# Kernel tuning notes

Measured on AMD Instinct MI355X. Metric: run time of the kernel, lower is better.

## Reference

```python
import jax, jax.numpy as jnp
import numpy as np

B, S, H = 2, 2048, 1024
NUM_HEAD = 16
HEAD = H // NUM_HEAD
NEG = -10000000000.0


def setup_inputs() -> dict:
    key = jax.random.key(0)
    ks = jax.random.split(key, 10)
    scale = 1.0 / np.sqrt(H)
    return {
        "query": jax.random.normal(ks[0], (B, S, H), jnp.float32),
        "key": jax.random.normal(ks[1], (B, S, H), jnp.float32),
        "value": jax.random.normal(ks[2], (B, S, H), jnp.float32),
        "mask": jax.random.randint(ks[3], (B, S), 0, 2, jnp.int32),
        "Wq": jax.random.normal(ks[4], (H, H), jnp.float32) * scale,
        "bq": jnp.zeros((H,), jnp.float32),
        "Wk": jax.random.normal(ks[5], (H, H), jnp.float32) * scale,
        "bk": jnp.zeros((H,), jnp.float32),
        "Wv": jax.random.normal(ks[6], (H, H), jnp.float32) * scale,
        "bv": jnp.zeros((H,), jnp.float32),
    }


def reference(query, key, value, mask, Wq, bq, Wk, bk, Wv, bv):
    b, s, h = query.shape
    # Linear projections (torch Linear: x @ W.T + b), split into heads -> [b, nh, s, hd]
    def proj(x, W, bias):
        y = x @ W.T + bias
        return y.reshape(b, s, NUM_HEAD, HEAD).transpose(0, 2, 1, 3)

    q = proj(query, Wq, bq)
    k = proj(key, Wk, bk)
    v = proj(value, Wv, bv)

    # NOTE: original module has NO 1/sqrt(head_dim) scaling -- faithful.
    attn_score = jnp.einsum("bhqd,bhkd->bhqk", q, k)  # [b, nh, s, s]
    # key-padding mask bias: 0 where mask==1, -1e10 where mask==0, broadcast over query dim
    bias_add = jnp.where(mask[:, None, None, :] == 0, NEG, 0.0).astype(attn_score.dtype)
    attn_score = attn_score + bias_add
    attn_ratio = jax.nn.softmax(attn_score, axis=-1)
    out = jnp.einsum("bhqk,bhkd->bhqd", attn_ratio, v)  # [b, nh, s, hd]
    out = out.transpose(0, 2, 1, 3).reshape(b, s, h)
    # Dropout is identity in eval mode; output_linear is defined but never used in forward.
    return out
```

## Files before the change

### kernel.cpp

```cpp
#include <hip/hip_runtime.h>

#define BATCH 2
#define S_LEN 2048
#define HDIM  1024
#define NHEAD 16
#define HD    64
#define NEGBIAS -1e10f

typedef __attribute__((ext_vector_type(8))) _Float16 half8;
typedef __attribute__((ext_vector_type(4))) _Float16 half4;
typedef __attribute__((ext_vector_type(4))) float   f32x4;

__global__ __launch_bounds__(256) void proj_gemm_f16(
    const float* __restrict__ Xq, const float* __restrict__ Wq, const float* __restrict__ bq,
    const float* __restrict__ Xk, const float* __restrict__ Wk, const float* __restrict__ bk,
    const float* __restrict__ Xv, const float* __restrict__ Wv, const float* __restrict__ bv,
    _Float16* __restrict__ Qb, _Float16* __restrict__ Kb, _Float16* __restrict__ Vtb)
{
    const int z = blockIdx.z;
    const float* X    = (z == 0) ? Xq : (z == 1) ? Xk : Xv;
    const float* W    = (z == 0) ? Wq : (z == 1) ? Wk : Wv;
    const float* bias = (z == 0) ? bq : (z == 1) ? bk : bv;
    _Float16* Y       = (z == 0) ? Qb : (z == 1) ? Kb : Vtb;

    const int n0 = blockIdx.x * 128;
    const int m0 = blockIdx.y * 128;

    __shared__ __align__(16) _Float16 As[128][40];
    __shared__ __align__(16) _Float16 Bs[128][40];

    const int t    = threadIdx.x;
    const int w    = t >> 6;
    const int lane = t & 63;
    const int quad = lane >> 4;
    const int lc   = lane & 15;
    const int wm   = (w >> 1) * 64;
    const int wn   = (w & 1) * 64;

    const f32x4 fzero = {0.f, 0.f, 0.f, 0.f};
    f32x4 acc[4][4];
#pragma unroll
    for (int i = 0; i < 4; i++)
#pragma unroll
        for (int j = 0; j < 4; j++) acc[i][j] = fzero;

    const int srow = t >> 2;
    const int sc   = t & 3;

    float4 xa[2][2], wa[2][2];
#define PROJ_ISSUE(K0)                                                        \
    {                                                                         \
        _Pragma("unroll")                                                     \
        for (int hf = 0; hf < 2; hf++) {                                      \
            const float* gx = X + (size_t)(m0 + srow + hf * 64) * HDIM + (K0) + sc * 8; \
            xa[hf][0] = *(const float4*)gx;                                   \
            xa[hf][1] = *(const float4*)(gx + 4);                             \
            const float* gw = W + (size_t)(n0 + srow + hf * 64) * HDIM + (K0) + sc * 8; \
            wa[hf][0] = *(const float4*)gw;                                   \
            wa[hf][1] = *(const float4*)(gw + 4);                             \
        }                                                                     \
    }

    PROJ_ISSUE(0)

    for (int k0 = 0; k0 < HDIM; k0 += 32) {
        if (k0) __syncthreads();
#pragma unroll
        for (int hf = 0; hf < 2; hf++) {
            int row = srow + hf * 64;
            half8 vx;
            vx[0] = (_Float16)xa[hf][0].x; vx[1] = (_Float16)xa[hf][0].y;
            vx[2] = (_Float16)xa[hf][0].z; vx[3] = (_Float16)xa[hf][0].w;
            vx[4] = (_Float16)xa[hf][1].x; vx[5] = (_Float16)xa[hf][1].y;
            vx[6] = (_Float16)xa[hf][1].z; vx[7] = (_Float16)xa[hf][1].w;
            *(half8*)&As[row][sc * 8] = vx;
            half8 vw;
            vw[0] = (_Float16)wa[hf][0].x; vw[1] = (_Float16)wa[hf][0].y;
            vw[2] = (_Float16)wa[hf][0].z; vw[3] = (_Float16)wa[hf][0].w;
            vw[4] = (_Float16)wa[hf][1].x; vw[5] = (_Float16)wa[hf][1].y;
            vw[6] = (_Float16)wa[hf][1].z; vw[7] = (_Float16)wa[hf][1].w;
            *(half8*)&Bs[row][sc * 8] = vw;
        }
        __syncthreads();

        if (k0 + 32 < HDIM) PROJ_ISSUE(k0 + 32)

        half8 af[4], bf[4];
#pragma unroll
        for (int mt = 0; mt < 4; mt++)
            af[mt] = *(const half8*)&As[wm + mt * 16 + lc][quad * 8];
#pragma unroll
        for (int nt = 0; nt < 4; nt++)
            bf[nt] = *(const half8*)&Bs[wn + nt * 16 + lc][quad * 8];
#pragma unroll
        for (int mt = 0; mt < 4; mt++)
#pragma unroll
            for (int nt = 0; nt < 4; nt++)
                acc[mt][nt] = __builtin_amdgcn_mfma_f32_16x16x32_f16(
                    af[mt], bf[nt], acc[mt][nt], 0, 0, 0);
    }

#pragma unroll
    for (int nt = 0; nt < 4; nt++) {
        const int n = n0 + wn + nt * 16 + lc;
        const float bv_ = bias[n];
        const int h = n >> 6, d = n & 63;
#pragma unroll
        for (int mt = 0; mt < 4; mt++) {
#pragma unroll
            for (int r = 0; r < 4; r++) {
                const int m = m0 + wm + mt * 16 + quad * 4 + r;
                const int b = m >> 11, s = m & (S_LEN - 1);
                const int bh = b * NHEAD + h;
                _Float16 val = (_Float16)(acc[mt][nt][r] + bv_);
                if (z == 2)
                    Y[((size_t)bh * HD + d) * S_LEN + s] = val;
                else
                    Y[((size_t)bh * S_LEN + s) * HD + d] = val;
            }
        }
    }
}

__global__ __launch_bounds__(256) void flash_attn_mfma(
    const _Float16* __restrict__ Qb, const _Float16* __restrict__ Kb,
    const _Float16* __restrict__ Vtb, const int* __restrict__ mask,
    float* __restrict__ out)
{
    const int qt = blockIdx.x & 15;
    const int bh = blockIdx.x >> 4;
    const int b  = bh >> 4;
    const int h  = bh & (NHEAD - 1);

    __shared__ __align__(16) _Float16 Ks [64][72];
    __shared__ __align__(16) _Float16 Vts[64][72];
    __shared__ __align__(16) _Float16 Ps [4][32][72];
    __shared__ float biasS[64];

    const int t    = threadIdx.x;
    const int w    = t >> 6;
    const int lane = t & 63;
    const int quad = lane >> 4;
    const int lc   = lane & 15;

    const _Float16* Kbase = Kb  + (size_t)bh * S_LEN * HD;
    const _Float16* Vbase = Vtb + (size_t)bh * HD * S_LEN;
    const int* mbase = mask + b * S_LEN;

    half8 qf[2][2];
#pragma unroll
    for (int qg = 0; qg < 2; qg++) {
        const int qrow = qt * 128 + w * 32 + qg * 16 + lc;
#pragma unroll
        for (int s = 0; s < 2; s++)
            qf[qg][s] = *(const half8*)(Qb + ((size_t)bh * S_LEN + qrow) * HD
                                        + s * 32 + quad * 8);
    }

    const f32x4 fzero = {0.f, 0.f, 0.f, 0.f};
    f32x4 o[2][4];
#pragma unroll
    for (int qg = 0; qg < 2; qg++)
#pragma unroll
        for (int nt = 0; nt < 4; nt++) o[qg][nt] = fzero;
    float mrun[2] = {-3.0e38f, -3.0e38f};
    float lrun[2] = {0.f, 0.f};

    const int rr0 = t >> 3,          cc0 = (t & 7) * 8;
    const int rr1 = (t + 256) >> 3,  cc1 = (t & 7) * 8;

    half8 kpre[2], vpre[2];
    int   mpre;
#define ATTN_ISSUE(KT)                                                        \
    {                                                                         \
        kpre[0] = *(const half8*)(Kbase + (size_t)((KT) + rr0) * HD + cc0);   \
        kpre[1] = *(const half8*)(Kbase + (size_t)((KT) + rr1) * HD + cc1);   \
        vpre[0] = *(const half8*)(Vbase + (size_t)rr0 * S_LEN + (KT) + cc0);  \
        vpre[1] = *(const half8*)(Vbase + (size_t)rr1 * S_LEN + (KT) + cc1);  \
        mpre    = mbase[(KT) + (t & 63)];                                     \
    }

    ATTN_ISSUE(0)

    for (int kt = 0; kt < S_LEN; kt += 64) {
        if (kt) __syncthreads();
        *(half8*)&Ks [rr0][cc0] = kpre[0];
        *(half8*)&Ks [rr1][cc1] = kpre[1];
        *(half8*)&Vts[rr0][cc0] = vpre[0];
        *(half8*)&Vts[rr1][cc1] = vpre[1];
        if (t < 64) biasS[t] = mpre ? 0.f : NEGBIAS;
        __syncthreads();

        if (kt + 64 < S_LEN) ATTN_ISSUE(kt + 64)

        f32x4 scf[2][4];
#pragma unroll
        for (int qg = 0; qg < 2; qg++)
#pragma unroll
            for (int tt = 0; tt < 4; tt++) scf[qg][tt] = fzero;
#pragma unroll
        for (int s = 0; s < 2; s++) {
#pragma unroll
            for (int tt = 0; tt < 4; tt++) {
                half8 kf = *(const half8*)&Ks[tt * 16 + lc][s * 32 + quad * 8];
                scf[0][tt] = __builtin_amdgcn_mfma_f32_16x16x32_f16(kf, qf[0][s], scf[0][tt], 0, 0, 0);
                scf[1][tt] = __builtin_amdgcn_mfma_f32_16x16x32_f16(kf, qf[1][s], scf[1][tt], 0, 0, 0);
            }
        }

#pragma unroll
        for (int tt = 0; tt < 4; tt++) {
            float4 b4 = *(const float4*)&biasS[tt * 16 + quad * 4];
#pragma unroll
            for (int qg = 0; qg < 2; qg++) {
                scf[qg][tt][0] += b4.x; scf[qg][tt][1] += b4.y;
                scf[qg][tt][2] += b4.z; scf[qg][tt][3] += b4.w;
            }
        }

#pragma unroll
        for (int qg = 0; qg < 2; qg++) {
            float mx = scf[qg][0][0];
#pragma unroll
            for (int tt = 0; tt < 4; tt++)
#pragma unroll
                for (int r = 0; r < 4; r++) mx = fmaxf(mx, scf[qg][tt][r]);
            mx = fmaxf(mx, __shfl_xor(mx, 16));
            mx = fmaxf(mx, __shfl_xor(mx, 32));

            float mn = fmaxf(mrun[qg], mx);
            float al = __expf(mrun[qg] - mn);
            float ls = 0.f;
#pragma unroll
            for (int tt = 0; tt < 4; tt++)
#pragma unroll
                for (int r = 0; r < 4; r++) {
                    float p = __expf(scf[qg][tt][r] - mn);
                    scf[qg][tt][r] = p;
                    ls += p;
                }
            ls += __shfl_xor(ls, 16);
            ls += __shfl_xor(ls, 32);
            lrun[qg] = lrun[qg] * al + ls;
            mrun[qg] = mn;
#pragma unroll
            for (int nt = 0; nt < 4; nt++) {
                o[qg][nt][0] *= al; o[qg][nt][1] *= al;
                o[qg][nt][2] *= al; o[qg][nt][3] *= al;
            }

#pragma unroll
            for (int tt = 0; tt < 4; tt++) {
                half4 pk;
                pk[0] = (_Float16)scf[qg][tt][0]; pk[1] = (_Float16)scf[qg][tt][1];
                pk[2] = (_Float16)scf[qg][tt][2]; pk[3] = (_Float16)scf[qg][tt][3];
                *(half4*)&Ps[w][qg * 16 + lc][tt * 16 + quad * 4] = pk;
            }
        }

#pragma unroll
        for (int s = 0; s < 2; s++) {
            half8 pf0 = *(const half8*)&Ps[w][lc]     [s * 32 + quad * 8];
            half8 pf1 = *(const half8*)&Ps[w][16 + lc][s * 32 + quad * 8];
#pragma unroll
            for (int nt = 0; nt < 4; nt++) {
                half8 vf = *(const half8*)&Vts[nt * 16 + lc][s * 32 + quad * 8];
                o[0][nt] = __builtin_amdgcn_mfma_f32_16x16x32_f16(vf, pf0, o[0][nt], 0, 0, 0);
                o[1][nt] = __builtin_amdgcn_mfma_f32_16x16x32_f16(vf, pf1, o[1][nt], 0, 0, 0);
            }
        }
    }

#pragma unroll
    for (int qg = 0; qg < 2; qg++) {
        const int qrow = qt * 128 + w * 32 + qg * 16 + lc;
        const float inv = 1.f / lrun[qg];
        const size_t rowb = ((size_t)b * S_LEN + qrow) * HDIM + h * HD;
#pragma unroll
        for (int nt = 0; nt < 4; nt++) {
            float4 v;
            v.x = o[qg][nt][0] * inv; v.y = o[qg][nt][1] * inv;
            v.z = o[qg][nt][2] * inv; v.w = o[qg][nt][3] * inv;
            *(float4*)&out[rowb + nt * 16 + quad * 4] = v;
        }
    }
}

extern "C" void kernel_launch(void* const* d_in, const int* in_sizes, int n_in,
                              void* d_out, int out_size, void* d_ws, size_t ws_size,
                              hipStream_t stream) {
    const float* query = (const float*)d_in[0];
    const float* key   = (const float*)d_in[1];
    const float* value = (const float*)d_in[2];
    const int*   mask  = (const int*)  d_in[3];
    const float* Wq    = (const float*)d_in[4];
    const float* bq    = (const float*)d_in[5];
    const float* Wk    = (const float*)d_in[6];
    const float* bk    = (const float*)d_in[7];
    const float* Wv    = (const float*)d_in[8];
    const float* bv    = (const float*)d_in[9];
    float* out = (float*)d_out;

    const size_t nElem = (size_t)BATCH * S_LEN * HDIM;
    if (ws_size < 3 * nElem * sizeof(_Float16)) return;
    _Float16* Qb  = (_Float16*)d_ws;
    _Float16* Kb  = Qb + nElem;
    _Float16* Vtb = Kb + nElem;

    dim3 gproj(HDIM / 128, (BATCH * S_LEN) / 128, 3);
    proj_gemm_f16<<<gproj, 256, 0, stream>>>(query, Wq, bq, key, Wk, bk,
                                             value, Wv, bv, Qb, Kb, Vtb);

    flash_attn_mfma<<<BATCH * NHEAD * (S_LEN / 128), 256, 0, stream>>>(
        Qb, Kb, Vtb, mask, out);
}
```

Measured before the change: 243.9 us.

## Use exp2 softmax with lazy rescale, swizzled LDS, and block remap in attention

Several changes land together. Q is pre-multiplied by log2(e) in the projection so softmax can use exp2f. The running-max rescale of o and l is skipped unless some row's max grows by more than 8 (a lazy rescale). The padded LDS tiles are replaced with XOR-swizzled 128-byte rows to avoid bank conflicts and save LDS. P is packed to fp16 with cvt_pkrtz, and block indices are remapped across heads. The lazy rescale lets P values reach up to 2^8 before conversion to fp16, which carries some precision risk.

```diff
diff --git a/kernel.cpp b/kernel.cpp
--- a/kernel.cpp
+++ b/kernel.cpp
@@ -6,6 +6,7 @@
 #define NHEAD 16
 #define HD    64
 #define NEGBIAS -1e10f
+#define LOG2E 1.44269504088896f
 
 typedef __attribute__((ext_vector_type(8))) _Float16 half8;
 typedef __attribute__((ext_vector_type(4))) _Float16 half4;
@@ -112,7 +113,9 @@
                 const int m = m0 + wm + mt * 16 + quad * 4 + r;
                 const int b = m >> 11, s = m & (S_LEN - 1);
                 const int bh = b * NHEAD + h;
-                _Float16 val = (_Float16)(acc[mt][nt][r] + bv_);
+                float y = acc[mt][nt][r] + bv_;
+                if (z == 0) y *= LOG2E;
+                _Float16 val = (_Float16)y;
                 if (z == 2)
                     Y[((size_t)bh * HD + d) * S_LEN + s] = val;
                 else
@@ -121,20 +124,25 @@
         }
     }
 }
+
+
+#define SWZB(row, cb) (((row) << 7) + ((cb) ^ (((row) & 7) << 4)))
 
 __global__ __launch_bounds__(256) void flash_attn_mfma(
     const _Float16* __restrict__ Qb, const _Float16* __restrict__ Kb,
     const _Float16* __restrict__ Vtb, const int* __restrict__ mask,
     float* __restrict__ out)
 {
-    const int qt = blockIdx.x & 15;
-    const int bh = blockIdx.x >> 4;
+    const int bid = blockIdx.x;
+    const int swz = (bid & 7) * 64 + (bid >> 3);
+    const int qt = swz & 15;
+    const int bh = swz >> 4;
     const int b  = bh >> 4;
     const int h  = bh & (NHEAD - 1);
 
-    __shared__ __align__(16) _Float16 Ks [64][72];
-    __shared__ __align__(16) _Float16 Vts[64][72];
-    __shared__ __align__(16) _Float16 Ps [4][32][72];
+    __shared__ __align__(16) _Float16 KsBuf [64 * 64];
+    __shared__ __align__(16) _Float16 VtsBuf[64 * 64];
+    __shared__ __align__(16) _Float16 PsBuf [4][32 * 64];
     __shared__ float biasS[64];
 
     const int t    = threadIdx.x;
@@ -143,6 +151,10 @@
     const int quad = lane >> 4;
     const int lc   = lane & 15;
 
+    char* KsB  = (char*)KsBuf;
+    char* VtsB = (char*)VtsBuf;
+    char* PsB  = (char*)PsBuf[w];
+
     const _Float16* Kbase = Kb  + (size_t)bh * S_LEN * HD;
     const _Float16* Vbase = Vtb + (size_t)bh * HD * S_LEN;
     const int* mbase = mask + b * S_LEN;
@@ -166,28 +178,28 @@
     float mrun[2] = {-3.0e38f, -3.0e38f};
     float lrun[2] = {0.f, 0.f};
 
-    const int rr0 = t >> 3,          cc0 = (t & 7) * 8;
-    const int rr1 = (t + 256) >> 3,  cc1 = (t & 7) * 8;
+    const int rr0 = t >> 3,          cb0 = (t & 7) * 16;
+    const int rr1 = (t + 256) >> 3;
 
     half8 kpre[2], vpre[2];
     int   mpre;
-#define ATTN_ISSUE(KT)                                                        \
-    {                                                                         \
-        kpre[0] = *(const half8*)(Kbase + (size_t)((KT) + rr0) * HD + cc0);   \
-        kpre[1] = *(const half8*)(Kbase + (size_t)((KT) + rr1) * HD + cc1);   \
-        vpre[0] = *(const half8*)(Vbase + (size_t)rr0 * S_LEN + (KT) + cc0);  \
-        vpre[1] = *(const half8*)(Vbase + (size_t)rr1 * S_LEN + (KT) + cc1);  \
-        mpre    = mbase[(KT) + (t & 63)];                                     \
+#define ATTN_ISSUE(KT)                                                          \
+    {                                                                           \
+        kpre[0] = *(const half8*)(Kbase + (size_t)((KT) + rr0) * HD + (cb0 >> 1)); \
+        kpre[1] = *(const half8*)(Kbase + (size_t)((KT) + rr1) * HD + (cb0 >> 1)); \
+        vpre[0] = *(const half8*)(Vbase + (size_t)rr0 * S_LEN + (KT) + (cb0 >> 1)); \
+        vpre[1] = *(const half8*)(Vbase + (size_t)rr1 * S_LEN + (KT) + (cb0 >> 1)); \
+        mpre    = mbase[(KT) + (t & 63)];                                       \
     }
 
     ATTN_ISSUE(0)
 
     for (int kt = 0; kt < S_LEN; kt += 64) {
         if (kt) __syncthreads();
-        *(half8*)&Ks [rr0][cc0] = kpre[0];
-        *(half8*)&Ks [rr1][cc1] = kpre[1];
-        *(half8*)&Vts[rr0][cc0] = vpre[0];
-        *(half8*)&Vts[rr1][cc1] = vpre[1];
+        *(half8*)(KsB  + SWZB(rr0, cb0)) = kpre[0];
+        *(half8*)(KsB  + SWZB(rr1, cb0)) = kpre[1];
+        *(half8*)(VtsB + SWZB(rr0, cb0)) = vpre[0];
+        *(half8*)(VtsB + SWZB(rr1, cb0)) = vpre[1];
         if (t < 64) biasS[t] = mpre ? 0.f : NEGBIAS;
         __syncthreads();
 
@@ -202,7 +214,7 @@
         for (int s = 0; s < 2; s++) {
 #pragma unroll
             for (int tt = 0; tt < 4; tt++) {
-                half8 kf = *(const half8*)&Ks[tt * 16 + lc][s * 32 + quad * 8];
+                half8 kf = *(const half8*)(KsB + SWZB(tt * 16 + lc, s * 64 + quad * 16));
                 scf[0][tt] = __builtin_amdgcn_mfma_f32_16x16x32_f16(kf, qf[0][s], scf[0][tt], 0, 0, 0);
                 scf[1][tt] = __builtin_amdgcn_mfma_f32_16x16x32_f16(kf, qf[1][s], scf[1][tt], 0, 0, 0);
             }
@@ -228,43 +240,47 @@
             mx = fmaxf(mx, __shfl_xor(mx, 16));
             mx = fmaxf(mx, __shfl_xor(mx, 32));
 
-            float mn = fmaxf(mrun[qg], mx);
-            float al = __expf(mrun[qg] - mn);
+            if (!__all(mx <= mrun[qg] + 8.f)) {
+                float mn = fmaxf(mrun[qg], mx);
+                float al = exp2f(mrun[qg] - mn);
+                lrun[qg] *= al;
+#pragma unroll
+                for (int nt = 0; nt < 4; nt++) {
+                    o[qg][nt][0] *= al; o[qg][nt][1] *= al;
+                    o[qg][nt][2] *= al; o[qg][nt][3] *= al;
+                }
+                mrun[qg] = mn;
+            }
+
             float ls = 0.f;
 #pragma unroll
             for (int tt = 0; tt < 4; tt++)
 #pragma unroll
                 for (int r = 0; r < 4; r++) {
-                    float p = __expf(scf[qg][tt][r] - mn);
+                    float p = exp2f(scf[qg][tt][r] - mrun[qg]);
                     scf[qg][tt][r] = p;
                     ls += p;
                 }
             ls += __shfl_xor(ls, 16);
             ls += __shfl_xor(ls, 32);
-            lrun[qg] = lrun[qg] * al + ls;
-            mrun[qg] = mn;
+            lrun[qg] += ls;
+
+#pragma unroll
+            for (int tt = 0; tt < 4; tt++) {
+                auto pk01 = __builtin_amdgcn_cvt_pkrtz(scf[qg][tt][0], scf[qg][tt][1]);
+                auto pk23 = __builtin_amdgcn_cvt_pkrtz(scf[qg][tt][2], scf[qg][tt][3]);
+                auto pk   = __builtin_shufflevector(pk01, pk23, 0, 1, 2, 3);
+                *(decltype(pk)*)(PsB + SWZB(qg * 16 + lc, tt * 32 + quad * 8)) = pk;
+            }
+        }
+
+#pragma unroll
+        for (int s = 0; s < 2; s++) {
+            half8 pf0 = *(const half8*)(PsB + SWZB(lc,      s * 64 + quad * 16));
+            half8 pf1 = *(const half8*)(PsB + SWZB(16 + lc, s * 64 + quad * 16));
 #pragma unroll
             for (int nt = 0; nt < 4; nt++) {
-                o[qg][nt][0] *= al; o[qg][nt][1] *= al;
-                o[qg][nt][2] *= al; o[qg][nt][3] *= al;
-            }
-
-#pragma unroll
-            for (int tt = 0; tt < 4; tt++) {
-                half4 pk;
-                pk[0] = (_Float16)scf[qg][tt][0]; pk[1] = (_Float16)scf[qg][tt][1];
-                pk[2] = (_Float16)scf[qg][tt][2]; pk[3] = (_Float16)scf[qg][tt][3];
-                *(half4*)&Ps[w][qg * 16 + lc][tt * 16 + quad * 4] = pk;
-            }
-        }
-
-#pragma unroll
-        for (int s = 0; s < 2; s++) {
-            half8 pf0 = *(const half8*)&Ps[w][lc]     [s * 32 + quad * 8];
-            half8 pf1 = *(const half8*)&Ps[w][16 + lc][s * 32 + quad * 8];
-#pragma unroll
-            for (int nt = 0; nt < 4; nt++) {
-                half8 vf = *(const half8*)&Vts[nt * 16 + lc][s * 32 + quad * 8];
+                half8 vf = *(const half8*)(VtsB + SWZB(nt * 16 + lc, s * 64 + quad * 16));
                 o[0][nt] = __builtin_amdgcn_mfma_f32_16x16x32_f16(vf, pf0, o[0][nt], 0, 0, 0);
                 o[1][nt] = __builtin_amdgcn_mfma_f32_16x16x32_f16(vf, pf1, o[1][nt], 0, 0, 0);
             }
```

After: 247.1 us. About the same (+1.3%).

## Use exp2 softmax with lazy rescaling, packed fp16 converts, and block swizzle

Applied to the files above, without the earlier changes.

Q is pre-scaled by log2(e) in the projection epilogue so the softmax can use hardware exp2 directly. The running-max rescale of the output accumulators is skipped unless some lane's max grows by more than 8, and the mask bias is folded into the MFMA accumulator initialisation. Float-to-half conversions now use packed round-toward-zero instructions, max reduction uses three-input max, and attention blocks are swizzled in their launch order. The lazy rescale allows partially stale maxima, which bounds exp2 inputs near 2^8 and relies on fp16 range. Round-toward-zero also changes rounding of the P values and the projection outputs.

```diff
diff --git a/kernel.cpp b/kernel.cpp
--- a/kernel.cpp
+++ b/kernel.cpp
@@ -6,10 +6,18 @@
 #define NHEAD 16
 #define HD    64
 #define NEGBIAS -1e10f
+#define LOG2E 1.44269504088896f
 
 typedef __attribute__((ext_vector_type(8))) _Float16 half8;
 typedef __attribute__((ext_vector_type(4))) _Float16 half4;
 typedef __attribute__((ext_vector_type(4))) float   f32x4;
+typedef __attribute__((ext_vector_type(2))) __fp16 fp16x2;
+typedef __attribute__((ext_vector_type(4))) __fp16 fp16x4;
+typedef __attribute__((ext_vector_type(8))) __fp16 fp16x8;
+
+__device__ __forceinline__ float max3f(float a, float b, float c) {
+    return fmaxf(fmaxf(a, b), c);
+}
 
 __global__ __launch_bounds__(256) void proj_gemm_f16(
     const float* __restrict__ Xq, const float* __restrict__ Wq, const float* __restrict__ bq,
@@ -61,6 +69,18 @@
         }                                                                     \
     }
 
+#define PK8(dst, f0, f1)                                                      \
+    {                                                                         \
+        fp16x2 p0 = __builtin_amdgcn_cvt_pkrtz((f0).x, (f0).y);               \
+        fp16x2 p1 = __builtin_amdgcn_cvt_pkrtz((f0).z, (f0).w);               \
+        fp16x2 p2 = __builtin_amdgcn_cvt_pkrtz((f1).x, (f1).y);               \
+        fp16x2 p3 = __builtin_amdgcn_cvt_pkrtz((f1).z, (f1).w);               \
+        fp16x4 lo = __builtin_shufflevector(p0, p1, 0, 1, 2, 3);              \
+        fp16x4 hi = __builtin_shufflevector(p2, p3, 0, 1, 2, 3);              \
+        fp16x8 v8 = __builtin_shufflevector(lo, hi, 0, 1, 2, 3, 4, 5, 6, 7);  \
+        dst = __builtin_bit_cast(half8, v8);                                  \
+    }
+
     PROJ_ISSUE(0)
 
     for (int k0 = 0; k0 < HDIM; k0 += 32) {
@@ -68,17 +88,10 @@
 #pragma unroll
         for (int hf = 0; hf < 2; hf++) {
             int row = srow + hf * 64;
-            half8 vx;
-            vx[0] = (_Float16)xa[hf][0].x; vx[1] = (_Float16)xa[hf][0].y;
-            vx[2] = (_Float16)xa[hf][0].z; vx[3] = (_Float16)xa[hf][0].w;
-            vx[4] = (_Float16)xa[hf][1].x; vx[5] = (_Float16)xa[hf][1].y;
-            vx[6] = (_Float16)xa[hf][1].z; vx[7] = (_Float16)xa[hf][1].w;
+            half8 vx, vw;
+            PK8(vx, xa[hf][0], xa[hf][1])
+            PK8(vw, wa[hf][0], wa[hf][1])
             *(half8*)&As[row][sc * 8] = vx;
-            half8 vw;
-            vw[0] = (_Float16)wa[hf][0].x; vw[1] = (_Float16)wa[hf][0].y;
-            vw[2] = (_Float16)wa[hf][0].z; vw[3] = (_Float16)wa[hf][0].w;
-            vw[4] = (_Float16)wa[hf][1].x; vw[5] = (_Float16)wa[hf][1].y;
-            vw[6] = (_Float16)wa[hf][1].z; vw[7] = (_Float16)wa[hf][1].w;
             *(half8*)&Bs[row][sc * 8] = vw;
         }
         __syncthreads();
@@ -112,7 +125,9 @@
                 const int m = m0 + wm + mt * 16 + quad * 4 + r;
                 const int b = m >> 11, s = m & (S_LEN - 1);
                 const int bh = b * NHEAD + h;
-                _Float16 val = (_Float16)(acc[mt][nt][r] + bv_);
+                float y = acc[mt][nt][r] + bv_;
+                if (z == 0) y *= LOG2E;
+                _Float16 val = (_Float16)y;
                 if (z == 2)
                     Y[((size_t)bh * HD + d) * S_LEN + s] = val;
                 else
@@ -127,8 +142,10 @@
     const _Float16* __restrict__ Vtb, const int* __restrict__ mask,
     float* __restrict__ out)
 {
-    const int qt = blockIdx.x & 15;
-    const int bh = blockIdx.x >> 4;
+    const int bid = blockIdx.x;
+    const int swz = (bid & 7) * 64 + (bid >> 3);
+    const int qt = swz & 15;
+    const int bh = swz >> 4;
     const int b  = bh >> 4;
     const int h  = bh & (NHEAD - 1);
 
@@ -157,8 +174,8 @@
                                         + s * 32 + quad * 8);
     }
 
+    f32x4 o[2][4];
     const f32x4 fzero = {0.f, 0.f, 0.f, 0.f};
-    f32x4 o[2][4];
 #pragma unroll
     for (int qg = 0; qg < 2; qg++)
 #pragma unroll
@@ -167,16 +184,16 @@
     float lrun[2] = {0.f, 0.f};
 
     const int rr0 = t >> 3,          cc0 = (t & 7) * 8;
-    const int rr1 = (t + 256) >> 3,  cc1 = (t & 7) * 8;
+    const int rr1 = (t + 256) >> 3;
 
     half8 kpre[2], vpre[2];
     int   mpre;
 #define ATTN_ISSUE(KT)                                                        \
     {                                                                         \
         kpre[0] = *(const half8*)(Kbase + (size_t)((KT) + rr0) * HD + cc0);   \
-        kpre[1] = *(const half8*)(Kbase + (size_t)((KT) + rr1) * HD + cc1);   \
+        kpre[1] = *(const half8*)(Kbase + (size_t)((KT) + rr1) * HD + cc0);   \
         vpre[0] = *(const half8*)(Vbase + (size_t)rr0 * S_LEN + (KT) + cc0);  \
-        vpre[1] = *(const half8*)(Vbase + (size_t)rr1 * S_LEN + (KT) + cc1);  \
+        vpre[1] = *(const half8*)(Vbase + (size_t)rr1 * S_LEN + (KT) + cc0);  \
         mpre    = mbase[(KT) + (t & 63)];                                     \
     }
 
@@ -185,9 +202,9 @@
     for (int kt = 0; kt < S_LEN; kt += 64) {
         if (kt) __syncthreads();
         *(half8*)&Ks [rr0][cc0] = kpre[0];
-        *(half8*)&Ks [rr1][cc1] = kpre[1];
+        *(half8*)&Ks [rr1][cc0] = kpre[1];
         *(half8*)&Vts[rr0][cc0] = vpre[0];
-        *(half8*)&Vts[rr1][cc1] = vpre[1];
+        *(half8*)&Vts[rr1][cc0] = vpre[1];
         if (t < 64) biasS[t] = mpre ? 0.f : NEGBIAS;
         __syncthreads();
 
@@ -195,9 +212,12 @@
 
         f32x4 scf[2][4];
 #pragma unroll
-        for (int qg = 0; qg < 2; qg++)
-#pragma unroll
-            for (int tt = 0; tt < 4; tt++) scf[qg][tt] = fzero;
+        for (int tt = 0; tt < 4; tt++) {
+            float4 b4 = *(const float4*)&biasS[tt * 16 + quad * 4];
+            f32x4 cini = {b4.x, b4.y, b4.z, b4.w};
+            scf[0][tt] = cini;
+            scf[1][tt] = cini;
+        }
 #pragma unroll
         for (int s = 0; s < 2; s++) {
 #pragma unroll
@@ -209,52 +229,55 @@
         }
 
 #pragma unroll
-        for (int tt = 0; tt < 4; tt++) {
-            float4 b4 = *(const float4*)&biasS[tt * 16 + quad * 4];
-#pragma unroll
-            for (int qg = 0; qg < 2; qg++) {
-                scf[qg][tt][0] += b4.x; scf[qg][tt][1] += b4.y;
-                scf[qg][tt][2] += b4.z; scf[qg][tt][3] += b4.w;
-            }
-        }
-
-#pragma unroll
         for (int qg = 0; qg < 2; qg++) {
-            float mx = scf[qg][0][0];
-#pragma unroll
-            for (int tt = 0; tt < 4; tt++)
-#pragma unroll
-                for (int r = 0; r < 4; r++) mx = fmaxf(mx, scf[qg][tt][r]);
+            const f32x4 a0 = scf[qg][0], a1 = scf[qg][1],
+                        a2 = scf[qg][2], a3 = scf[qg][3];
+            float m0 = max3f(a0[0], a0[1], a0[2]);
+            float m1 = max3f(a0[3], a1[0], a1[1]);
+            float m2 = max3f(a1[2], a1[3], a2[0]);
+            float m3 = max3f(a2[1], a2[2], a2[3]);
+            float m4 = max3f(a3[0], a3[1], a3[2]);
+            float mx = fmaxf(max3f(m0, m1, m2), max3f(m3, m4, a3[3]));
             mx = fmaxf(mx, __shfl_xor(mx, 16));
             mx = fmaxf(mx, __shfl_xor(mx, 32));
 
-            float mn = fmaxf(mrun[qg], mx);
-            float al = __expf(mrun[qg] - mn);
-            float ls = 0.f;
+            if (!__all(mx <= mrun[qg] + 8.f)) {
+                float mn = fmaxf(mrun[qg], mx);
+                float al = __builtin_amdgcn_exp2f(mrun[qg] - mn);
+                lrun[qg] *= al;
+#pragma unroll
+                for (int nt = 0; nt < 4; nt++) {
+                    o[qg][nt][0] *= al; o[qg][nt][1] *= al;
+                    o[qg][nt][2] *= al; o[qg][nt][3] *= al;
+                }
+                mrun[qg] = mn;
+            }
+
+            const float mr = mrun[qg];
+            float ps[4][4];
 #pragma unroll
             for (int tt = 0; tt < 4; tt++)
 #pragma unroll
                 for (int r = 0; r < 4; r++) {
-                    float p = __expf(scf[qg][tt][r] - mn);
-                    scf[qg][tt][r] = p;
-                    ls += p;
+                    float p = __builtin_amdgcn_exp2f(scf[qg][tt][r] - mr);
+                    ps[tt][r] = p;
                 }
+            float s0 = (ps[0][0] + ps[0][1]) + (ps[0][2] + ps[0][3]);
+            float s1 = (ps[1][0] + ps[1][1]) + (ps[1][2] + ps[1][3]);
+            float s2 = (ps[2][0] + ps[2][1]) + (ps[2][2] + ps[2][3]);
+            float s3 = (ps[3][0] + ps[3][1]) + (ps[3][2] + ps[3][3]);
+            float ls = (s0 + s1) + (s2 + s3);
             ls += __shfl_xor(ls, 16);
             ls += __shfl_xor(ls, 32);
-            lrun[qg] = lrun[qg] * al + ls;
-            mrun[qg] = mn;
-#pragma unroll
-            for (int nt = 0; nt < 4; nt++) {
-                o[qg][nt][0] *= al; o[qg][nt][1] *= al;
-                o[qg][nt][2] *= al; o[qg][nt][3] *= al;
-            }
+            lrun[qg] += ls;
 
 #pragma unroll
             for (int tt = 0; tt < 4; tt++) {
-                half4 pk;
-                pk[0] = (_Float16)scf[qg][tt][0]; pk[1] = (_Float16)scf[qg][tt][1];
-                pk[2] = (_Float16)scf[qg][tt][2]; pk[3] = (_Float16)scf[qg][tt][3];
-                *(half4*)&Ps[w][qg * 16 + lc][tt * 16 + quad * 4] = pk;
+                fp16x2 p01 = __builtin_amdgcn_cvt_pkrtz(ps[tt][0], ps[tt][1]);
+                fp16x2 p23 = __builtin_amdgcn_cvt_pkrtz(ps[tt][2], ps[tt][3]);
+                fp16x4 pk4 = __builtin_shufflevector(p01, p23, 0, 1, 2, 3);
+                *(half4*)&Ps[w][qg * 16 + lc][tt * 16 + quad * 4] =
+                    __builtin_bit_cast(half4, pk4);
             }
         }
 
```

Result: faster. 234.4 us (-3.9%).
